# Performance work log

Measured on AMD Instinct MI355X. Metric: run time of the kernel, lower is better.

The kernel has to match this reference:

```python
import jax, jax.numpy as jnp
import numpy as np

SHAPELET_SIZE = 64
NUM_SHAPELETS = 128
IN_CHANNELS = 8


def setup_inputs() -> dict:
    key = jax.random.key(0)
    k1, k2 = jax.random.split(key)
    x = jax.random.normal(k1, (64, IN_CHANNELS, 2048), dtype=jnp.float32)
    shapelets = jax.random.normal(k2, (IN_CHANNELS, NUM_SHAPELETS, SHAPELET_SIZE), dtype=jnp.float32)
    return {"x": x, "shapelets": shapelets}


def _znorm(s):
    # Z-normalize along the time-step axis (dim 2), matching Znormalize_dim(shapelets, 2)
    mu = jnp.mean(s, axis=2, keepdims=True)
    sd = jnp.std(s, axis=2, keepdims=True)
    return (s - mu) / sd


def reference(x, shapelets):
    # x: (N, C, L); shapelets: (C, K, S)
    S = shapelets.shape[-1]
    N, C, L = x.shape
    W = L - S + 1
    # unfold(2, S, 1): sliding windows -> (N, C, W, S)
    idx = jnp.arange(W)[:, None] + jnp.arange(S)[None, :]  # (W, S)
    xw = x[:, :, idx]  # (N, C, W, S)
    sh = _znorm(shapelets)  # (C, K, S)
    # Euclidean cdist via ||a||^2 + ||b||^2 - 2 a.b (avoids (N,C,W,K,S) blowup)
    sq_x = jnp.sum(xw * xw, axis=-1)          # (N, C, W)
    sq_s = jnp.sum(sh * sh, axis=-1)          # (C, K)
    cross = jnp.einsum('ncws,cks->ncwk', xw, sh)  # (N, C, W, K)
    d2 = sq_x[..., None] + sq_s[None, :, None, :] - 2.0 * cross
    d = jnp.sqrt(jnp.maximum(d2, 1e-12))      # (N, C, W, K)
    # sum over channels, then global min over windows -> (N, 1, K)
    dsum = jnp.sum(d, axis=1)                 # (N, W, K)
    out = jnp.min(dsum, axis=1)[:, None, :]   # (N, 1, K)
    return out
```

## Files before the change

### kernel.cpp

```cpp
#include <hip/hip_runtime.h>
#include <hip/hip_bf16.h>
#include <math.h>

#define C 8
#define K 128
#define S 64
#define L 2048
#define NB 64
#define W (L - S + 1)
#define TW 128
#define NTW 16
#define NKB 2
#define XCS 208
#define XFS 200

typedef __attribute__((ext_vector_type(8))) short bf16x8;
typedef __attribute__((ext_vector_type(4))) float f32x4;

__device__ __forceinline__ unsigned short f2bf(float f) {
  unsigned int u = __float_as_uint(f);
  u += 0x7FFFu + ((u >> 16) & 1u);
  return (unsigned short)(u >> 16);
}

__device__ __forceinline__ unsigned int pkbf(float a, float b) {
  __hip_bfloat162 h = __float22bfloat162_rn(make_float2(a, b));
  return *reinterpret_cast<unsigned int*>(&h);
}

__device__ __forceinline__ void gll16(const void* g, void* l) {
  __builtin_amdgcn_global_load_lds((const __attribute__((address_space(1))) void*)g,
                                   (__attribute__((address_space(3))) void*)l, 16, 0, 0);
}

__global__ __launch_bounds__(256) void prep_kernel(const float* __restrict__ sh,
                                                   unsigned short* __restrict__ shzB,
                                                   float* __restrict__ out) {
  int tid = blockIdx.x * 256 + threadIdx.x;
  if (tid < NB * K) out[tid] = __int_as_float(0x7F800000);
  int gid = blockIdx.x * 4 + (threadIdx.x >> 6);
  int lane = threadIdx.x & 63;
  float v = sh[(size_t)gid * S + lane];
  float s1 = v, s2 = v * v;
#pragma unroll
  for (int off = 32; off > 0; off >>= 1) {
    s1 += __shfl_down(s1, off);
    s2 += __shfl_down(s2, off);
  }
  s1 = __shfl(s1, 0);
  s2 = __shfl(s2, 0);
  float mu = s1 * (1.0f / S);
  float sd = sqrtf(fmaxf(s2 * (1.0f / S) - mu * mu, 0.0f));
  float z = (v - mu) / sd;
  int c = gid >> 7, k = gid & (K - 1), s = lane;
  int idx = (k >> 6) * 32768 + c * 4096 + ((((k >> 4) & 3) * 2) + (s >> 5)) * 512 +
            ((((s >> 3) & 3) * 16 + (k & 15)) * 8) + (s & 7);
  shzB[idx] = f2bf(-2.0f * z);
}

__global__ __launch_bounds__(512, 4) void main_kernel(const float* __restrict__ x,
                                                      const unsigned short* __restrict__ shzB,
                                                      int* __restrict__ out) {
  __shared__ __align__(16) unsigned short bbuf[4096];
  __shared__ __align__(16) unsigned short xcop[C][8][XCS];
  __shared__ __align__(16) float sqx[C][TW];

  const int t = threadIdx.x;
  const int lane = t & 63;
  const int wave = t >> 6;
  const int wgrp = wave & 1;
  const int kgrp = wave >> 1;
  const int col = lane & 15;
  const int quad = lane >> 4;
  const int n = blockIdx.z;
  const int kblk = blockIdx.y;
  const int w0 = blockIdx.x * TW;
  const float* xn = x + (size_t)n * C * L;
  const unsigned short* bsrc = shzB + kblk * 32768;

  float* xf = (float*)bbuf;
  {
    const int c = wave;
    const int e = lane * 4;
    float4 v; v.x = v.y = v.z = v.w = 0.0f;
    if (lane < 48) {
      int g = w0 + e;
      if (g + 3 < L) {
        v = *(const float4*)(xn + c * L + g);
      } else {
        v.x = (g + 0 < L) ? xn[c * L + g + 0] : 0.0f;
        v.y = (g + 1 < L) ? xn[c * L + g + 1] : 0.0f;
        v.z = (g + 2 < L) ? xn[c * L + g + 2] : 0.0f;
        v.w = (g + 3 < L) ? xn[c * L + g + 3] : 0.0f;
      }
    }
    if (lane < 50) *(float4*)&xf[c * XFS + e] = v;
  }
  __syncthreads();

  {
    const int cb = wave;
    const int rb = lane >> 3;
    const int c8 = lane & 7;
    const float* xr = xf + cb * XFS;
#pragma unroll
    for (int j = 0; j < 12; ++j) {
      int i = (c8 + j * 8) * 2;
      *(unsigned int*)&xcop[cb][rb][i] = pkbf(xr[i + rb], xr[i + rb + 1]);
    }
  }
  {
    const int c = wave, wl = lane * 2;
    const float* xr = xf + c * XFS;
    float p0 = 0.f, p1 = 0.f, p2 = 0.f, p3 = 0.f;
#pragma unroll
    for (int si = 0; si < S; si += 4) {
      float v0 = xr[wl + si], v1 = xr[wl + si + 1], v2 = xr[wl + si + 2], v3 = xr[wl + si + 3];
      p0 = fmaf(v0, v0, p0); p1 = fmaf(v1, v1, p1);
      p2 = fmaf(v2, v2, p2); p3 = fmaf(v3, v3, p3);
    }
    float s0 = 64.0f + (p0 + p1) + (p2 + p3);
    sqx[c][wl] = s0;
    float a = xr[wl + S], b = xr[wl];
    sqx[c][wl + 1] = s0 + a * a - b * b;
  }
  __syncthreads();

  gll16(bsrc + t * 8, &bbuf[wave * 512]);

  const f32x4 z4 = {0.0f, 0.0f, 0.0f, 0.0f};
  f32x4 dsum[4];
#pragma unroll
  for (int a = 0; a < 4; ++a) dsum[a] = z4;

  const int r8 = col & 7;
  const int abase = wgrp * 64 + (col - r8) + quad * 8;

  for (int c = 0; c < C; ++c) {
    __syncthreads();
    bf16x8 b0 = *(const bf16x8*)(&bbuf[(kgrp * 2 + 0) * 512 + lane * 8]);
    bf16x8 b1 = *(const bf16x8*)(&bbuf[(kgrp * 2 + 1) * 512 + lane * 8]);
    __syncthreads();

    if (c + 1 < C)
      gll16(bsrc + (c + 1) * 4096 + t * 8, &bbuf[wave * 512]);

    f32x4 acc[4];
#pragma unroll
    for (int wt = 0; wt < 4; ++wt)
      acc[wt] = *(const f32x4*)&sqx[c][wgrp * 64 + wt * 16 + quad * 4];
    const unsigned short* xc = &xcop[c][r8][0];
#pragma unroll
    for (int wt = 0; wt < 4; ++wt) {
      bf16x8 a0 = *(const bf16x8*)(xc + abase + wt * 16);
      acc[wt] = __builtin_amdgcn_mfma_f32_16x16x32_bf16(a0, b0, acc[wt], 0, 0, 0);
    }
#pragma unroll
    for (int wt = 0; wt < 4; ++wt) {
      bf16x8 a1 = *(const bf16x8*)(xc + abase + wt * 16 + 32);
      acc[wt] = __builtin_amdgcn_mfma_f32_16x16x32_bf16(a1, b1, acc[wt], 0, 0, 0);
    }
#pragma unroll
    for (int wt = 0; wt < 4; ++wt)
#pragma unroll
      for (int i = 0; i < 4; ++i)
        dsum[wt][i] += __builtin_amdgcn_sqrtf(fmaxf(acc[wt][i], 0.0f));
  }

  const float INF = __int_as_float(0x7F800000);
  int wbase = w0 + wgrp * 64;
  float mv = INF;
#pragma unroll
  for (int wt = 0; wt < 4; ++wt)
#pragma unroll
    for (int i = 0; i < 4; ++i) {
      int w = wbase + wt * 16 + quad * 4 + i;
      mv = (w < W) ? fminf(mv, dsum[wt][i]) : mv;
    }
  mv = fminf(mv, __shfl_xor(mv, 16));
  mv = fminf(mv, __shfl_xor(mv, 32));
  if (quad == 0)
    atomicMin(&out[n * K + kblk * 64 + kgrp * 16 + col], __float_as_int(mv));
}

extern "C" void kernel_launch(void* const* d_in, const int* in_sizes, int n_in,
                              void* d_out, int out_size, void* d_ws, size_t ws_size,
                              hipStream_t stream) {
  const float* x = (const float*)d_in[0];
  const float* sh = (const float*)d_in[1];
  float* out = (float*)d_out;
  unsigned short* shzB = (unsigned short*)d_ws;

  prep_kernel<<<256, 256, 0, stream>>>(sh, shzB, out);
  main_kernel<<<dim3(NTW, NKB, NB), 512, 0, stream>>>(x, shzB, (int*)out);
}
```

Before: 91.43 us.

## Process all 128 shapelets per block instead of splitting K across two blocks

Drops the K-block grid dimension so each block computes all 128 shapelets, with each wave handling two 16-wide K tiles that share the A fragments. This halves the redundant loading of x, the bf16 conversion and the sqx computation that were repeated per K block. The shapelet layout in prep is changed to match. In exchange the grid halves (1024 blocks), the LDS buffer for B doubles, per-thread registers grow, and the occupancy hint in launch bounds is removed.

```diff
diff --git a/kernel.cpp b/kernel.cpp
--- a/kernel.cpp
+++ b/kernel.cpp
@@ -10,7 +10,6 @@
 #define W (L - S + 1)
 #define TW 128
 #define NTW 16
-#define NKB 2
 #define XCS 208
 #define XFS 200
 
@@ -53,15 +52,15 @@
   float sd = sqrtf(fmaxf(s2 * (1.0f / S) - mu * mu, 0.0f));
   float z = (v - mu) / sd;
   int c = gid >> 7, k = gid & (K - 1), s = lane;
-  int idx = (k >> 6) * 32768 + c * 4096 + ((((k >> 4) & 3) * 2) + (s >> 5)) * 512 +
+  int idx = c * 8192 + ((k >> 4) * 2 + (s >> 5)) * 512 +
             ((((s >> 3) & 3) * 16 + (k & 15)) * 8) + (s & 7);
   shzB[idx] = f2bf(-2.0f * z);
 }
 
-__global__ __launch_bounds__(512, 4) void main_kernel(const float* __restrict__ x,
-                                                      const unsigned short* __restrict__ shzB,
-                                                      int* __restrict__ out) {
-  __shared__ __align__(16) unsigned short bbuf[4096];
+__global__ __launch_bounds__(512) void main_kernel(const float* __restrict__ x,
+                                                   const unsigned short* __restrict__ shzB,
+                                                   int* __restrict__ out) {
+  __shared__ __align__(16) unsigned short bbuf[8192];
   __shared__ __align__(16) unsigned short xcop[C][8][XCS];
   __shared__ __align__(16) float sqx[C][TW];
 
@@ -72,11 +71,9 @@
   const int kgrp = wave >> 1;
   const int col = lane & 15;
   const int quad = lane >> 4;
-  const int n = blockIdx.z;
-  const int kblk = blockIdx.y;
+  const int n = blockIdx.y;
   const int w0 = blockIdx.x * TW;
   const float* xn = x + (size_t)n * C * L;
-  const unsigned short* bsrc = shzB + kblk * 32768;
 
   float* xf = (float*)bbuf;
   {
@@ -126,61 +123,79 @@
   }
   __syncthreads();
 
-  gll16(bsrc + t * 8, &bbuf[wave * 512]);
+#pragma unroll
+  for (int i = 0; i < 2; ++i)
+    gll16(shzB + i * 4096 + t * 8, &bbuf[i * 4096 + wave * 512]);
 
   const f32x4 z4 = {0.0f, 0.0f, 0.0f, 0.0f};
-  f32x4 dsum[4];
-#pragma unroll
-  for (int a = 0; a < 4; ++a) dsum[a] = z4;
+  f32x4 dsum[4][2];
+#pragma unroll
+  for (int a = 0; a < 4; ++a)
+#pragma unroll
+    for (int b = 0; b < 2; ++b) dsum[a][b] = z4;
 
   const int r8 = col & 7;
   const int abase = wgrp * 64 + (col - r8) + quad * 8;
 
   for (int c = 0; c < C; ++c) {
     __syncthreads();
-    bf16x8 b0 = *(const bf16x8*)(&bbuf[(kgrp * 2 + 0) * 512 + lane * 8]);
-    bf16x8 b1 = *(const bf16x8*)(&bbuf[(kgrp * 2 + 1) * 512 + lane * 8]);
+    bf16x8 bfr[2][2];
+#pragma unroll
+    for (int ks = 0; ks < 2; ++ks)
+#pragma unroll
+      for (int kt = 0; kt < 2; ++kt)
+        bfr[ks][kt] = *(const bf16x8*)(&bbuf[((kgrp * 2 + kt) * 2 + ks) * 512 + lane * 8]);
     __syncthreads();
 
-    if (c + 1 < C)
-      gll16(bsrc + (c + 1) * 4096 + t * 8, &bbuf[wave * 512]);
-
-    f32x4 acc[4];
+    if (c + 1 < C) {
+#pragma unroll
+      for (int i = 0; i < 2; ++i)
+        gll16(shzB + (c + 1) * 8192 + i * 4096 + t * 8, &bbuf[i * 4096 + wave * 512]);
+    }
+
+    f32x4 acc[4][2];
+#pragma unroll
+    for (int wt = 0; wt < 4; ++wt) {
+      f32x4 sx = *(const f32x4*)&sqx[c][wgrp * 64 + wt * 16 + quad * 4];
+      acc[wt][0] = sx;
+      acc[wt][1] = sx;
+    }
+    const unsigned short* xc = &xcop[c][r8][0];
+#pragma unroll
+    for (int ks = 0; ks < 2; ++ks) {
+#pragma unroll
+      for (int wt = 0; wt < 4; ++wt) {
+        bf16x8 af = *(const bf16x8*)(xc + abase + wt * 16 + ks * 32);
+        acc[wt][0] = __builtin_amdgcn_mfma_f32_16x16x32_bf16(af, bfr[ks][0], acc[wt][0], 0, 0, 0);
+        acc[wt][1] = __builtin_amdgcn_mfma_f32_16x16x32_bf16(af, bfr[ks][1], acc[wt][1], 0, 0, 0);
+      }
+    }
 #pragma unroll
     for (int wt = 0; wt < 4; ++wt)
-      acc[wt] = *(const f32x4*)&sqx[c][wgrp * 64 + wt * 16 + quad * 4];
-    const unsigned short* xc = &xcop[c][r8][0];
-#pragma unroll
-    for (int wt = 0; wt < 4; ++wt) {
-      bf16x8 a0 = *(const bf16x8*)(xc + abase + wt * 16);
-      acc[wt] = __builtin_amdgcn_mfma_f32_16x16x32_bf16(a0, b0, acc[wt], 0, 0, 0);
-    }
-#pragma unroll
-    for (int wt = 0; wt < 4; ++wt) {
-      bf16x8 a1 = *(const bf16x8*)(xc + abase + wt * 16 + 32);
-      acc[wt] = __builtin_amdgcn_mfma_f32_16x16x32_bf16(a1, b1, acc[wt], 0, 0, 0);
-    }
-#pragma unroll
-    for (int wt = 0; wt < 4; ++wt)
-#pragma unroll
-      for (int i = 0; i < 4; ++i)
-        dsum[wt][i] += __builtin_amdgcn_sqrtf(fmaxf(acc[wt][i], 0.0f));
+#pragma unroll
+      for (int kt = 0; kt < 2; ++kt)
+#pragma unroll
+        for (int i = 0; i < 4; ++i)
+          dsum[wt][kt][i] += __builtin_amdgcn_sqrtf(fmaxf(acc[wt][kt][i], 0.0f));
   }
 
   const float INF = __int_as_float(0x7F800000);
   int wbase = w0 + wgrp * 64;
-  float mv = INF;
-#pragma unroll
-  for (int wt = 0; wt < 4; ++wt)
-#pragma unroll
-    for (int i = 0; i < 4; ++i) {
-      int w = wbase + wt * 16 + quad * 4 + i;
-      mv = (w < W) ? fminf(mv, dsum[wt][i]) : mv;
-    }
-  mv = fminf(mv, __shfl_xor(mv, 16));
-  mv = fminf(mv, __shfl_xor(mv, 32));
-  if (quad == 0)
-    atomicMin(&out[n * K + kblk * 64 + kgrp * 16 + col], __float_as_int(mv));
+#pragma unroll
+  for (int kt = 0; kt < 2; ++kt) {
+    float mv = INF;
+#pragma unroll
+    for (int wt = 0; wt < 4; ++wt)
+#pragma unroll
+      for (int i = 0; i < 4; ++i) {
+        int w = wbase + wt * 16 + quad * 4 + i;
+        mv = (w < W) ? fminf(mv, dsum[wt][kt][i]) : mv;
+      }
+    mv = fminf(mv, __shfl_xor(mv, 16));
+    mv = fminf(mv, __shfl_xor(mv, 32));
+    if (quad == 0)
+      atomicMin(&out[n * K + kgrp * 32 + kt * 16 + col], __float_as_int(mv));
+  }
 }
 
 extern "C" void kernel_launch(void* const* d_in, const int* in_sizes, int n_in,
@@ -192,5 +207,5 @@
   unsigned short* shzB = (unsigned short*)d_ws;
 
   prep_kernel<<<256, 256, 0, stream>>>(sh, shzB, out);
-  main_kernel<<<dim3(NTW, NKB, NB), 512, 0, stream>>>(x, shzB, (int*)out);
-}
+  main_kernel<<<dim3(NTW, NB), 512, 0, stream>>>(x, shzB, (int*)out);
+}
```

After: 173.0 us. 89.2% more time.
